# Optimization experiments

Hardware: AMD Instinct MI355X
Metric: run time of the kernel (lower is better)

Reference implementation:

```python
import jax, jax.numpy as jnp
import numpy as np

N = 4096        # nodes
C = 256         # in_channels
E0 = 65536      # edges before adding self-loops
RATIO = 0.5
K = int(np.ceil(RATIO * N))   # pooled nodes (topk)
NEG = 0.2       # leaky relu negative slope


def setup_inputs() -> dict:
    key = jax.random.key(0)
    ks = jax.random.split(key, 12)
    x = jax.random.normal(ks[0], (N, C), jnp.float32)
    src = jax.random.randint(ks[1], (E0,), 0, N)
    off = jax.random.randint(ks[2], (E0,), 1, N)
    dst = (src + off) % N                      # guaranteed no self-loops
    edge_index = jnp.stack([src, dst]).astype(jnp.int32)
    s = 1.0 / np.sqrt(C)
    s2 = 1.0 / np.sqrt(2 * C)
    u = lambda k, shape, b: jax.random.uniform(k, shape, jnp.float32, -b, b)
    return dict(
        x=x, edge_index=edge_index,
        Wq=u(ks[3], (C, C), s), bq=u(ks[4], (C,), s),          # lin_q
        gat_w=u(ks[5], (2 * C,), s2), gat_b=u(ks[6], (1,), s2),  # gat_att
        le1_w=u(ks[7], (C,), s), le1_b=u(ks[8], (1,), s),      # LEConv lin1
        le2_w=u(ks[9], (C,), s),                                # LEConv lin2 (no bias)
        le3_w=u(ks[10], (C,), s), le3_b=u(ks[11], (1,), s),    # LEConv lin3
    )


def _asap(x, edge_index, Wq, bq, gat_w, gat_b, le1_w, le1_b, le2_w, le3_w, le3_b):
    # add_remaining_self_loops (inputs have none -> all N loops, weight 1)
    loops = jnp.arange(N, dtype=edge_index.dtype)
    ei = jnp.concatenate([edge_index, jnp.stack([loops, loops])], axis=1)
    i, j = ei[0], ei[1]          # i: aggregation target, j: neighbor

    x_pool = x                   # GNN is None -> x_pool = x
    xj = x_pool[j]               # [E, C]

    # Master2Token attention: X_q = scatter_max over target i
    Xq = jax.ops.segment_max(xj, i, num_segments=N)       # [N, C]
    Mq = Xq @ Wq + bq                                     # lin_q
    sc = jnp.concatenate([Mq[i], xj], axis=-1) @ gat_w + gat_b[0]  # [E]
    sc = jnp.where(sc > 0, sc, NEG * sc)                  # leaky relu

    # segment softmax over targets i
    m = jax.ops.segment_max(sc, i, num_segments=N)
    e = jnp.exp(sc - m[i])
    z = jax.ops.segment_sum(e, i, num_segments=N)
    score = e / z[i]                                      # dropout_att=0, eval

    # cluster representation
    out = jax.ops.segment_sum(x[j] * score[:, None], i, num_segments=N)  # [N, C]

    # fitness = sigmoid(LEConv(out)): x_i' = lin3(x_i) + sum_j (lin1(x_j) - lin2(x_i))
    a = out @ le1_w + le1_b[0]                            # [N]
    b = out @ le2_w                                       # [N]
    agg = jax.ops.segment_sum(a[j] - b[i], i, num_segments=N)
    fitness = jax.nn.sigmoid(agg + out @ le3_w + le3_b[0])  # [N]

    # topk pooling (single graph -> global top_k)
    fit_k, perm = jax.lax.top_k(fitness, K)
    x_out = out[perm] * fit_k[:, None]                    # [K, C]

    # graph_connectivity: E = S^T A S (dense stand-in for coalesce+spspmm)
    n_idx = jnp.zeros(N, jnp.int32).at[perm].set(jnp.arange(K, dtype=jnp.int32))
    in_perm = jnp.zeros(N, bool).at[perm].set(True)
    sS = jax.lax.stop_gradient(score) * in_perm[i]        # score.detach(), kept-cluster edges
    S = jnp.zeros((N, K), x.dtype).at[j, n_idx[i]].add(sS)   # S[j, new(i)] = score
    A = jnp.zeros((N, N), x.dtype).at[i, j].add(1.0)      # edge_weight None -> ones, coalesced
    Eadj = S.T @ (A @ S)                                  # [K, K]
    # remove_self_loops then add_remaining_self_loops(fill=1)
    Eadj = Eadj - jnp.diag(jnp.diag(Eadj)) + jnp.eye(K, dtype=Eadj.dtype)
    return x_out, Eadj, perm


def reference(x, edge_index, Wq, bq, gat_w, gat_b, le1_w, le1_b, le2_w, le3_w, le3_b):
    return _asap(x, edge_index, Wq, bq, gat_w, gat_b,
                 le1_w, le1_b, le2_w, le3_w, le3_b)
```

## Files before the change

### kernel.cpp

```cpp
#include <hip/hip_runtime.h>
#include <math.h>

constexpr int NN  = 4096;
constexpr int CC  = 256;
constexpr int EE0 = 65536;
constexpr int EE  = 69632;
constexpr int KK  = 2048;
constexpr int SL  = 128;

__device__ __forceinline__ void edge_ij(const int* __restrict__ ei, int e, int& i, int& j) {
    if (e < EE0) { i = ei[e]; j = ei[EE0 + e]; }
    else         { i = e - EE0; j = i; }
}

__global__ __launch_bounds__(256) void k_build(const int* __restrict__ ei,
                                               int* cnt_i, int* cnt_j,
                                               int* lsti_j, int* slot_ij, int* lstj_i,
                                               const float* __restrict__ x,
                                               const float* __restrict__ Wq, const float* __restrict__ bq,
                                               const float* __restrict__ gat_w, const float* __restrict__ gat_b,
                                               double* wv, double* consts, double* beta_node, int EB) {
    const int t = threadIdx.x, g = t >> 6, l = t & 63;
    if ((int)blockIdx.x < EB) {
        int e = blockIdx.x * 256 + t;
        if (e >= EE) return;
        int i, j; edge_ij(ei, e, i, j);
        int si = atomicAdd(&cnt_i[i], 1);
        int sj = atomicAdd(&cnt_j[j], 1);
        lsti_j[i * SL + si]  = j;
        slot_ij[i * SL + si] = j * SL + sj;
        lstj_i[j * SL + sj]  = i;
        return;
    }
    if ((int)blockIdx.x < EB + CC) {
        int k = blockIdx.x - EB;
        double s = (double)Wq[k * CC + t] * (double)gat_w[t];
        #pragma unroll
        for (int d = 32; d > 0; d >>= 1) s += __shfl_down(s, d, 64);
        __shared__ double red[4];
        if (l == 0) red[g] = s;
        __syncthreads();
        if (t == 0) wv[k] = red[0] + red[1] + red[2] + red[3];
        if (k == 0 && t == 0) {
            double cb = 0.0;
            for (int q = 0; q < CC; ++q) cb += (double)bq[q] * (double)gat_w[q];
            consts[0] = cb + (double)gat_b[0];
        }
        return;
    }
    int m = (blockIdx.x - EB - CC) * 4 + g;
    const float* gw2 = gat_w + CC;
    float4 v = ((const float4*)(x + (size_t)m * CC))[l];
    double s = (double)v.x * (double)gw2[4 * l]     + (double)v.y * (double)gw2[4 * l + 1]
             + (double)v.z * (double)gw2[4 * l + 2] + (double)v.w * (double)gw2[4 * l + 3];
    #pragma unroll
    for (int d = 32; d > 0; d >>= 1) s += __shfl_down(s, d, 64);
    if (l == 0) beta_node[m] = s;
}

__global__ __launch_bounds__(256) void k_attn(const float* __restrict__ x,
                                              const int* __restrict__ cnt_i, const int* __restrict__ lsti_j,
                                              const int* __restrict__ slot_ij,
                                              const int* __restrict__ cnt_j, const int* __restrict__ lstj_i,
                                              const double* __restrict__ wv, const double* __restrict__ beta_node,
                                              const double* __restrict__ consts,
                                              const float* __restrict__ le1_w, const float* __restrict__ le1_b,
                                              const float* __restrict__ le2_w,
                                              const float* __restrict__ le3_w, const float* __restrict__ le3_b,
                                              float* __restrict__ sval_i, float* __restrict__ svalj,
                                              float* __restrict__ out32,
                                              double* __restrict__ zlog) {
    const int n = (blockIdx.x << 2) + (threadIdx.x >> 6);
    const int l = threadIdx.x & 63;
    const int base = n * SL;
    const int deg = cnt_i[n];

    int j0 = 0, j1 = 0;
    double b0 = 0.0, b1 = 0.0;
    if (l < deg)      { j0 = lsti_j[base + l];      b0 = beta_node[j0]; }
    if (l + 64 < deg) { j1 = lsti_j[base + l + 64]; b1 = beta_node[j1]; }

    float4 mx = make_float4(-INFINITY, -INFINITY, -INFINITY, -INFINITY);
    for (int p4 = 0; p4 < deg; p4 += 4) {
        {   int p = p4;
            int jp = __shfl(p < 64 ? j0 : j1, p & 63, 64);
            float4 v = ((const float4*)(x + (size_t)jp * CC))[l];
            mx.x = fmaxf(mx.x, v.x); mx.y = fmaxf(mx.y, v.y);
            mx.z = fmaxf(mx.z, v.z); mx.w = fmaxf(mx.w, v.w);
        }
        if (p4 + 1 < deg) { int p = p4 + 1;
            int jp = __shfl(p < 64 ? j0 : j1, p & 63, 64);
            float4 v = ((const float4*)(x + (size_t)jp * CC))[l];
            mx.x = fmaxf(mx.x, v.x); mx.y = fmaxf(mx.y, v.y);
            mx.z = fmaxf(mx.z, v.z); mx.w = fmaxf(mx.w, v.w);
        }
        if (p4 + 2 < deg) { int p = p4 + 2;
            int jp = __shfl(p < 64 ? j0 : j1, p & 63, 64);
            float4 v = ((const float4*)(x + (size_t)jp * CC))[l];
            mx.x = fmaxf(mx.x, v.x); mx.y = fmaxf(mx.y, v.y);
            mx.z = fmaxf(mx.z, v.z); mx.w = fmaxf(mx.w, v.w);
        }
        if (p4 + 3 < deg) { int p = p4 + 3;
            int jp = __shfl(p < 64 ? j0 : j1, p & 63, 64);
            float4 v = ((const float4*)(x + (size_t)jp * CC))[l];
            mx.x = fmaxf(mx.x, v.x); mx.y = fmaxf(mx.y, v.y);
            mx.z = fmaxf(mx.z, v.z); mx.w = fmaxf(mx.w, v.w);
        }
    }

    double al = (double)mx.x * wv[4 * l]     + (double)mx.y * wv[4 * l + 1]
              + (double)mx.z * wv[4 * l + 2] + (double)mx.w * wv[4 * l + 3];
    #pragma unroll
    for (int d = 32; d > 0; d >>= 1) al += __shfl_down(al, d, 64);
    double an = __shfl(al, 0, 64) + consts[0];

    double s0 = 0.0, s1 = 0.0;
    if (l < deg)      { double v = an + b0; s0 = v > 0.0 ? v : 0.2 * v; }
    if (l + 64 < deg) { double v = an + b1; s1 = v > 0.0 ? v : 0.2 * v; }
    double mm = -1e300;
    if (l < deg)      mm = fmax(mm, s0);
    if (l + 64 < deg) mm = fmax(mm, s1);
    #pragma unroll
    for (int d = 32; d > 0; d >>= 1) mm = fmax(mm, __shfl_xor(mm, d, 64));
    double z = 0.0;
    if (l < deg)      z += exp(s0 - mm);
    if (l + 64 < deg) z += exp(s1 - mm);
    #pragma unroll
    for (int d = 32; d > 0; d >>= 1) z += __shfl_xor(z, d, 64);
    double inv = 1.0 / z;

    double sc0 = 0.0, sc1 = 0.0;
    if (l < deg) {
        sc0 = exp(s0 - mm) * inv;
        float scf = (float)sc0;
        sval_i[base + l] = scf;
        svalj[slot_ij[base + l]] = scf;
    }
    if (l + 64 < deg) {
        sc1 = exp(s1 - mm) * inv;
        float scf = (float)sc1;
        sval_i[base + l + 64] = scf;
        svalj[slot_ij[base + l + 64]] = scf;
    }

    double A0x = 0, A0y = 0, A0z = 0, A0w = 0;
    double A1x = 0, A1y = 0, A1z = 0, A1w = 0;
    double A2x = 0, A2y = 0, A2z = 0, A2w = 0;
    double A3x = 0, A3y = 0, A3z = 0, A3w = 0;
    for (int p4 = 0; p4 < deg; p4 += 4) {
        {   int p = p4;
            double sc = __shfl(p < 64 ? sc0 : sc1, p & 63, 64);
            int jp = __shfl(p < 64 ? j0 : j1, p & 63, 64);
            float4 v = ((const float4*)(x + (size_t)jp * CC))[l];
            A0x += sc * (double)v.x; A0y += sc * (double)v.y;
            A0z += sc * (double)v.z; A0w += sc * (double)v.w;
        }
        if (p4 + 1 < deg) { int p = p4 + 1;
            double sc = __shfl(p < 64 ? sc0 : sc1, p & 63, 64);
            int jp = __shfl(p < 64 ? j0 : j1, p & 63, 64);
            float4 v = ((const float4*)(x + (size_t)jp * CC))[l];
            A1x += sc * (double)v.x; A1y += sc * (double)v.y;
            A1z += sc * (double)v.z; A1w += sc * (double)v.w;
        }
        if (p4 + 2 < deg) { int p = p4 + 2;
            double sc = __shfl(p < 64 ? sc0 : sc1, p & 63, 64);
            int jp = __shfl(p < 64 ? j0 : j1, p & 63, 64);
            float4 v = ((const float4*)(x + (size_t)jp * CC))[l];
            A2x += sc * (double)v.x; A2y += sc * (double)v.y;
            A2z += sc * (double)v.z; A2w += sc * (double)v.w;
        }
        if (p4 + 3 < deg) { int p = p4 + 3;
            double sc = __shfl(p < 64 ? sc0 : sc1, p & 63, 64);
            int jp = __shfl(p < 64 ? j0 : j1, p & 63, 64);
            float4 v = ((const float4*)(x + (size_t)jp * CC))[l];
            A3x += sc * (double)v.x; A3y += sc * (double)v.y;
            A3z += sc * (double)v.z; A3w += sc * (double)v.w;
        }
    }
    double o0 = A0x + A1x + A2x + A3x;
    double o1 = A0y + A1y + A2y + A3y;
    double o2 = A0z + A1z + A2z + A3z;
    double o3 = A0w + A1w + A2w + A3w;

    float4 ov; ov.x = (float)o0; ov.y = (float)o1; ov.z = (float)o2; ov.w = (float)o3;
    ((float4*)(out32 + (size_t)n * CC))[l] = ov;

    float4 w1 = ((const float4*)le1_w)[l];
    float4 w2 = ((const float4*)le2_w)[l];
    float4 w3 = ((const float4*)le3_w)[l];
    double t1 = o0 * (double)w1.x + o1 * (double)w1.y + o2 * (double)w1.z + o3 * (double)w1.w;
    double t2 = o0 * (double)w2.x + o1 * (double)w2.y + o2 * (double)w2.z + o3 * (double)w2.w;
    double t3 = o0 * (double)w3.x + o1 * (double)w3.y + o2 * (double)w3.z + o3 * (double)w3.w;
    #pragma unroll
    for (int d = 32; d > 0; d >>= 1) {
        t1 += __shfl_down(t1, d, 64);
        t2 += __shfl_down(t2, d, 64);
        t3 += __shfl_down(t3, d, 64);
    }
    double a64n;
    if (l == 0) {
        double a64_ = t1 + (double)le1_b[0];
        double b64_ = t2;
        double l3v_ = t3 + (double)le3_b[0];
        atomicAdd(&zlog[n], l3v_ - (double)deg * b64_);
        a64n = a64_;
    }
    a64n = __shfl(a64n, 0, 64);

    int cj = cnt_j[n], jb = n * SL;
    for (int p = l; p < cj; p += 64) {
        atomicAdd(&zlog[lstj_i[jb + p]], a64n);
    }
}

__global__ __launch_bounds__(256) void k_rank(const double* __restrict__ zlog,
                                              const float* __restrict__ out32,
                                              int* __restrict__ perm, int* __restrict__ n_idx,
                                              float* __restrict__ xout, float* __restrict__ operm) {
    int n = blockIdx.x, t = threadIdx.x;
    double zn = zlog[n];
    int cnt = 0;
    #pragma unroll
    for (int u = 0; u < NN / 256; ++u) {
        int m = t + u * 256;
        double zm = zlog[m];
        cnt += ((zm > zn) || (zm == zn && m < n)) ? 1 : 0;
    }
    #pragma unroll
    for (int d = 32; d > 0; d >>= 1) cnt += __shfl_down(cnt, d, 64);
    __shared__ int red[4];
    __shared__ int rr;
    if ((t & 63) == 0) red[t >> 6] = cnt;
    __syncthreads();
    if (t == 0) {
        int r = red[0] + red[1] + red[2] + red[3];
        rr = r;
        if (r < KK) {
            perm[r] = n;
            n_idx[n] = r;
            operm[r] = (float)n;
        } else {
            n_idx[n] = -1;
        }
    }
    __syncthreads();
    int r = rr;
    if (r < KK) {
        double fit = 1.0 / (1.0 + exp(-zn));
        xout[(size_t)r * CC + t] = (float)((double)out32[(size_t)n * CC + t] * fit);
    }
}

__global__ __launch_bounds__(256) void k_eadj(const int* __restrict__ cnt_i, const int* __restrict__ lsti_j,
                                              const float* __restrict__ sval_i,
                                              const int* __restrict__ cnt_j, const int* __restrict__ lstj_i,
                                              const float* __restrict__ svalj,
                                              const int* __restrict__ n_idx,
                                              const int* __restrict__ perm,
                                              float* __restrict__ Ead) {
    __shared__ float row[KK];
    int r = blockIdx.x, t = threadIdx.x;
    float4 z4 = make_float4(0.f, 0.f, 0.f, 0.f);
    for (int c = t; c < KK / 4; c += 256) ((float4*)row)[c] = z4;
    __syncthreads();
    int n = perm[r];
    int deg = cnt_i[n];
    int base = n * SL;
    int grp = t >> 5, lane = t & 31;
    for (int p = grp; p < deg; p += 8) {
        int j = lsti_j[base + p];
        float s1 = sval_i[base + p];
        int cj = cnt_j[j], jb = j * SL;
        for (int q = lane; q < cj; q += 32) {
            int c = n_idx[lstj_i[jb + q]];
            if (c >= 0) atomicAdd(&row[c], s1 * svalj[jb + q]);
        }
    }
    __syncthreads();
    float* __restrict__ erow = Ead + (size_t)r * KK;
    for (int c4 = t; c4 < KK / 4; c4 += 256) {
        float4 v = ((float4*)row)[c4];
        int base4 = c4 * 4;
        int dr = r - base4;
        if (dr >= 0 && dr < 4) ((float*)&v)[dr] = 1.0f;
        ((float4*)erow)[c4] = v;
    }
}

extern "C" void kernel_launch(void* const* d_in, const int* in_sizes, int n_in,
                              void* d_out, int out_size, void* d_ws, size_t ws_size,
                              hipStream_t stream) {
    const float* x     = (const float*)d_in[0];
    const int*   ei    = (const int*)d_in[1];
    const float* Wq    = (const float*)d_in[2];
    const float* bq    = (const float*)d_in[3];
    const float* gat_w = (const float*)d_in[4];
    const float* gat_b = (const float*)d_in[5];
    const float* le1_w = (const float*)d_in[6];
    const float* le1_b = (const float*)d_in[7];
    const float* le2_w = (const float*)d_in[8];
    const float* le3_w = (const float*)d_in[9];
    const float* le3_b = (const float*)d_in[10];

    float* xout  = (float*)d_out;
    float* Ead   = xout + (size_t)KK * CC;
    float* operm = Ead + (size_t)KK * KK;

    char* w = (char*)d_ws;
    auto alloc = [&](size_t bytes) -> void* {
        void* p = (void*)w;
        w += (bytes + 255) & ~(size_t)255;
        return p;
    };
    int*    cnt_i  = (int*)alloc(NN * 4);
    int*    cnt_j  = (int*)alloc(NN * 4);
    double* zlog   = (double*)alloc(NN * 8);
    float*  out32  = (float*)alloc((size_t)NN * CC * 4);
    double* beta_node = (double*)alloc(NN * 8);
    double* wv     = (double*)alloc(CC * 8);
    double* consts = (double*)alloc(64);
    int*   lsti_j  = (int*)alloc((size_t)NN * SL * 4);
    int*   slot_ij = (int*)alloc((size_t)NN * SL * 4);
    int*   lstj_i  = (int*)alloc((size_t)NN * SL * 4);
    float* sval_i  = (float*)alloc((size_t)NN * SL * 4);
    float* svalj   = (float*)alloc((size_t)NN * SL * 4);
    int*   n_idx   = (int*)alloc(NN * 4);
    int*   perm    = (int*)alloc(KK * 4);

    hipMemsetAsync(cnt_i, 0, 2 * NN * 4 + NN * 8, stream);

    const int EB = (EE + 255) / 256;

    k_build<<<EB + CC + NN / 4, 256, 0, stream>>>(ei, cnt_i, cnt_j,
                                                  lsti_j, slot_ij, lstj_i, x,
                                                  Wq, bq, gat_w, gat_b, wv, consts, beta_node, EB);
    k_attn<<<NN / 4, 256, 0, stream>>>(x, cnt_i, lsti_j, slot_ij, cnt_j, lstj_i,
                                       wv, beta_node, consts,
                                       le1_w, le1_b, le2_w, le3_w, le3_b,
                                       sval_i, svalj, out32, zlog);
    k_rank<<<NN, 256, 0, stream>>>(zlog, out32, perm, n_idx, xout, operm);
    k_eadj<<<KK, 256, 0, stream>>>(cnt_i, lsti_j, sval_i, cnt_j, lstj_i, svalj,
                                   n_idx, perm, Ead);
}
```

Before: 144.4 us.

## Replace workspace memset with self-resetting device globals and batch rank computation

Counters and the fitness accumulator move into device globals that later kernels zero for the next invocation, removing the separate memset launch. Degree counts are copied to workspace so the counters can be cleared early. The rank kernel stages all fitness values in LDS and has each block rank 16 nodes, which cuts global rereads but reduces the grid to 256 blocks with a serial per-node loop. Correctness depends on globals starting at zero and on no concurrent invocations.

Result: slower. 166.7 us (+15.4%).

```diff
diff --git a/kernel.cpp b/kernel.cpp
--- a/kernel.cpp
+++ b/kernel.cpp
@@ -8,13 +8,16 @@
 constexpr int KK  = 2048;
 constexpr int SL  = 128;
 
+__device__ int    g_cnt_i[NN];
+__device__ int    g_cnt_j[NN];
+__device__ double g_zlog[NN];
+
 __device__ __forceinline__ void edge_ij(const int* __restrict__ ei, int e, int& i, int& j) {
     if (e < EE0) { i = ei[e]; j = ei[EE0 + e]; }
     else         { i = e - EE0; j = i; }
 }
 
 __global__ __launch_bounds__(256) void k_build(const int* __restrict__ ei,
-                                               int* cnt_i, int* cnt_j,
                                                int* lsti_j, int* slot_ij, int* lstj_i,
                                                const float* __restrict__ x,
                                                const float* __restrict__ Wq, const float* __restrict__ bq,
@@ -25,8 +28,8 @@
         int e = blockIdx.x * 256 + t;
         if (e >= EE) return;
         int i, j; edge_ij(ei, e, i, j);
-        int si = atomicAdd(&cnt_i[i], 1);
-        int sj = atomicAdd(&cnt_j[j], 1);
+        int si = atomicAdd(&g_cnt_i[i], 1);
+        int sj = atomicAdd(&g_cnt_j[j], 1);
         lsti_j[i * SL + si]  = j;
         slot_ij[i * SL + si] = j * SL + sj;
         lstj_i[j * SL + sj]  = i;
@@ -59,9 +62,9 @@
 }
 
 __global__ __launch_bounds__(256) void k_attn(const float* __restrict__ x,
-                                              const int* __restrict__ cnt_i, const int* __restrict__ lsti_j,
+                                              const int* __restrict__ lsti_j,
                                               const int* __restrict__ slot_ij,
-                                              const int* __restrict__ cnt_j, const int* __restrict__ lstj_i,
+                                              const int* __restrict__ lstj_i,
                                               const double* __restrict__ wv, const double* __restrict__ beta_node,
                                               const double* __restrict__ consts,
                                               const float* __restrict__ le1_w, const float* __restrict__ le1_b,
@@ -69,11 +72,13 @@
                                               const float* __restrict__ le3_w, const float* __restrict__ le3_b,
                                               float* __restrict__ sval_i, float* __restrict__ svalj,
                                               float* __restrict__ out32,
-                                              double* __restrict__ zlog) {
+                                              int* __restrict__ deg_i, int* __restrict__ deg_j) {
     const int n = (blockIdx.x << 2) + (threadIdx.x >> 6);
     const int l = threadIdx.x & 63;
     const int base = n * SL;
-    const int deg = cnt_i[n];
+    const int deg = g_cnt_i[n];
+    const int cj  = g_cnt_j[n];
+    if (l == 0) { deg_i[n] = deg; deg_j[n] = cj; }
 
     int j0 = 0, j1 = 0;
     double b0 = 0.0, b1 = 0.0;
@@ -202,75 +207,90 @@
         double a64_ = t1 + (double)le1_b[0];
         double b64_ = t2;
         double l3v_ = t3 + (double)le3_b[0];
-        atomicAdd(&zlog[n], l3v_ - (double)deg * b64_);
+        atomicAdd(&g_zlog[n], l3v_ - (double)deg * b64_);
         a64n = a64_;
     }
     a64n = __shfl(a64n, 0, 64);
 
-    int cj = cnt_j[n], jb = n * SL;
+    int jb = n * SL;
     for (int p = l; p < cj; p += 64) {
-        atomicAdd(&zlog[lstj_i[jb + p]], a64n);
-    }
-}
-
-__global__ __launch_bounds__(256) void k_rank(const double* __restrict__ zlog,
-                                              const float* __restrict__ out32,
+        atomicAdd(&g_zlog[lstj_i[jb + p]], a64n);
+    }
+}
+
+__global__ __launch_bounds__(256) void k_rank(const float* __restrict__ out32,
                                               int* __restrict__ perm, int* __restrict__ n_idx,
                                               float* __restrict__ xout, float* __restrict__ operm) {
-    int n = blockIdx.x, t = threadIdx.x;
-    double zn = zlog[n];
-    int cnt = 0;
-    #pragma unroll
-    for (int u = 0; u < NN / 256; ++u) {
-        int m = t + u * 256;
-        double zm = zlog[m];
-        cnt += ((zm > zn) || (zm == zn && m < n)) ? 1 : 0;
-    }
-    #pragma unroll
-    for (int d = 32; d > 0; d >>= 1) cnt += __shfl_down(cnt, d, 64);
+    __shared__ double zl[NN];
     __shared__ int red[4];
     __shared__ int rr;
-    if ((t & 63) == 0) red[t >> 6] = cnt;
+    const int t = threadIdx.x, b = blockIdx.x;
+
+    if (t < 16) {
+        g_cnt_i[b * 16 + t] = 0;
+        g_cnt_j[b * 16 + t] = 0;
+    }
+    for (int u = t; u < NN; u += 256) zl[u] = g_zlog[u];
     __syncthreads();
-    if (t == 0) {
-        int r = red[0] + red[1] + red[2] + red[3];
-        rr = r;
+
+    for (int v = 0; v < 16; ++v) {
+        int n = b * 16 + v;
+        double zn = zl[n];
+        int cnt = 0;
+        #pragma unroll
+        for (int u = 0; u < NN / 256; ++u) {
+            int m = t + u * 256;
+            double zm = zl[m];
+            cnt += ((zm > zn) || (zm == zn && m < n)) ? 1 : 0;
+        }
+        #pragma unroll
+        for (int d = 32; d > 0; d >>= 1) cnt += __shfl_down(cnt, d, 64);
+        if ((t & 63) == 0) red[t >> 6] = cnt;
+        __syncthreads();
+        if (t == 0) {
+            int r = red[0] + red[1] + red[2] + red[3];
+            rr = r;
+            if (r < KK) {
+                perm[r] = n;
+                n_idx[n] = r;
+                operm[r] = (float)n;
+            } else {
+                n_idx[n] = -1;
+            }
+        }
+        __syncthreads();
+        int r = rr;
         if (r < KK) {
-            perm[r] = n;
-            n_idx[n] = r;
-            operm[r] = (float)n;
-        } else {
-            n_idx[n] = -1;
-        }
-    }
-    __syncthreads();
-    int r = rr;
-    if (r < KK) {
-        double fit = 1.0 / (1.0 + exp(-zn));
-        xout[(size_t)r * CC + t] = (float)((double)out32[(size_t)n * CC + t] * fit);
-    }
-}
-
-__global__ __launch_bounds__(256) void k_eadj(const int* __restrict__ cnt_i, const int* __restrict__ lsti_j,
+            double fit = 1.0 / (1.0 + exp(-zn));
+            xout[(size_t)r * CC + t] = (float)((double)out32[(size_t)n * CC + t] * fit);
+        }
+        __syncthreads();
+    }
+}
+
+__global__ __launch_bounds__(256) void k_eadj(const int* __restrict__ deg_i, const int* __restrict__ lsti_j,
                                               const float* __restrict__ sval_i,
-                                              const int* __restrict__ cnt_j, const int* __restrict__ lstj_i,
+                                              const int* __restrict__ deg_j, const int* __restrict__ lstj_i,
                                               const float* __restrict__ svalj,
                                               const int* __restrict__ n_idx,
                                               const int* __restrict__ perm,
                                               float* __restrict__ Ead) {
     __shared__ float row[KK];
     int r = blockIdx.x, t = threadIdx.x;
+
+    if (r < 512 && t < 8) g_zlog[r * 8 + t] = 0.0;
+
     float4 z4 = make_float4(0.f, 0.f, 0.f, 0.f);
     for (int c = t; c < KK / 4; c += 256) ((float4*)row)[c] = z4;
     __syncthreads();
     int n = perm[r];
-    int deg = cnt_i[n];
+    int deg = deg_i[n];
     int base = n * SL;
     int grp = t >> 5, lane = t & 31;
     for (int p = grp; p < deg; p += 8) {
         int j = lsti_j[base + p];
         float s1 = sval_i[base + p];
-        int cj = cnt_j[j], jb = j * SL;
+        int cj = deg_j[j], jb = j * SL;
         for (int q = lane; q < cj; q += 32) {
             int c = n_idx[lstj_i[jb + q]];
             if (c >= 0) atomicAdd(&row[c], s1 * svalj[jb + q]);
@@ -312,9 +332,6 @@
         w += (bytes + 255) & ~(size_t)255;
         return p;
     };
-    int*    cnt_i  = (int*)alloc(NN * 4);
-    int*    cnt_j  = (int*)alloc(NN * 4);
-    double* zlog   = (double*)alloc(NN * 8);
     float*  out32  = (float*)alloc((size_t)NN * CC * 4);
     double* beta_node = (double*)alloc(NN * 8);
     double* wv     = (double*)alloc(CC * 8);
@@ -326,19 +343,18 @@
     float* svalj   = (float*)alloc((size_t)NN * SL * 4);
     int*   n_idx   = (int*)alloc(NN * 4);
     int*   perm    = (int*)alloc(KK * 4);
-
-    hipMemsetAsync(cnt_i, 0, 2 * NN * 4 + NN * 8, stream);
+    int*   deg_i   = (int*)alloc(NN * 4);
+    int*   deg_j   = (int*)alloc(NN * 4);
 
     const int EB = (EE + 255) / 256;
 
-    k_build<<<EB + CC + NN / 4, 256, 0, stream>>>(ei, cnt_i, cnt_j,
-                                                  lsti_j, slot_ij, lstj_i, x,
+    k_build<<<EB + CC + NN / 4, 256, 0, stream>>>(ei, lsti_j, slot_ij, lstj_i, x,
                                                   Wq, bq, gat_w, gat_b, wv, consts, beta_node, EB);
-    k_attn<<<NN / 4, 256, 0, stream>>>(x, cnt_i, lsti_j, slot_ij, cnt_j, lstj_i,
+    k_attn<<<NN / 4, 256, 0, stream>>>(x, lsti_j, slot_ij, lstj_i,
                                        wv, beta_node, consts,
                                        le1_w, le1_b, le2_w, le3_w, le3_b,
-                                       sval_i, svalj, out32, zlog);
-    k_rank<<<NN, 256, 0, stream>>>(zlog, out32, perm, n_idx, xout, operm);
-    k_eadj<<<KK, 256, 0, stream>>>(cnt_i, lsti_j, sval_i, cnt_j, lstj_i, svalj,
+                                       sval_i, svalj, out32, deg_i, deg_j);
+    k_rank<<<256, 256, 0, stream>>>(out32, perm, n_idx, xout, operm);
+    k_eadj<<<KK, 256, 0, stream>>>(deg_i, lsti_j, sval_i, deg_j, lstj_i, svalj,
                                    n_idx, perm, Ead);
 }
```
